# Kernel optimization log

Hardware: AMD Instinct MI355X
Metric: run time of the kernel (lower is better)

## Reference

```python
import jax, jax.numpy as jnp
import numpy as np

EMB_DIM = 1024
HEAD_DIM = 64
NUM_HEADS = EMB_DIM // HEAD_DIM  # 16
BATCH = 2
SEQ = 2048


def setup_inputs() -> dict:
    key = jax.random.key(0)
    ks = jax.random.split(key, 8)
    s = 0.02
    return {
        "q": jax.random.normal(ks[0], (BATCH, SEQ, EMB_DIM), dtype=jnp.float32),
        "k": jax.random.normal(ks[1], (BATCH, SEQ, EMB_DIM), dtype=jnp.float32),
        "v": jax.random.normal(ks[2], (BATCH, SEQ, EMB_DIM), dtype=jnp.float32),
        "W_q": jax.random.normal(ks[3], (HEAD_DIM, HEAD_DIM), dtype=jnp.float32) * s,
        "W_k": jax.random.normal(ks[4], (HEAD_DIM, HEAD_DIM), dtype=jnp.float32) * s,
        "W_v": jax.random.normal(ks[5], (HEAD_DIM, HEAD_DIM), dtype=jnp.float32) * s,
        "W_fc": jax.random.normal(ks[6], (EMB_DIM, EMB_DIM), dtype=jnp.float32) * s,
        "b_fc": jax.random.normal(ks[7], (EMB_DIM,), dtype=jnp.float32) * s,
    }


def reference(q, k, v, W_q, W_k, W_v, W_fc, b_fc):
    b = v.shape[0]
    # split into heads: [B, S, H, D]
    qh = q.reshape(b, -1, NUM_HEADS, HEAD_DIM)
    kh = k.reshape(b, -1, NUM_HEADS, HEAD_DIM)
    vh = v.reshape(b, -1, NUM_HEADS, HEAD_DIM)
    # per-head shared projections (nn.Linear: x @ W.T, no bias)
    qh = jnp.einsum('bshd,ed->bshe', qh, W_q)
    kh = jnp.einsum('bshd,ed->bshe', kh, W_k)
    vh = jnp.einsum('bshd,ed->bshe', vh, W_v)
    # scores: [B, Q, K, H]
    attn = jnp.einsum('nqhd,nkhd->nqkh', qh, kh)
    # NOTE (faithful to source): softmax over the HEADS axis (dim=3),
    # and scale by sqrt(emb_dim), not sqrt(head_dim).
    attn = jax.nn.softmax(attn / jnp.sqrt(jnp.float32(EMB_DIM)), axis=3)
    # weighted values: [B, Q, H, D] -> [B, Q, EMB]
    out = jnp.einsum('nqkh,nkhd->nqhd', attn, vh).reshape(b, -1, EMB_DIM)
    return out @ W_fc.T + b_fc
```

## Files before the change

kernel.cpp:

```cpp
#include <hip/hip_runtime.h>
#include <hip/hip_bf16.h>

#define S_LEN 2048
#define NHEAD 16
#define HDIM 64
#define EMB 1024

typedef short v8s __attribute__((ext_vector_type(8)));
typedef float v4f __attribute__((ext_vector_type(4)));

__device__ __forceinline__ float bflo(unsigned u) {
    union { unsigned u; float f; } v; v.u = u << 16; return v.f;
}
__device__ __forceinline__ float bfhi(unsigned u) {
    union { unsigned u; float f; } v; v.u = u & 0xFFFF0000u; return v.f;
}
__device__ __forceinline__ unsigned cvtpk(float lo, float hi) {
    union { __hip_bfloat162 h2; unsigned u; } v;
    float2 f; f.x = lo; f.y = hi;
    v.h2 = __float22bfloat162_rn(f);
    return v.u;
}
__device__ __forceinline__ unsigned short f2bf(float f) {
    return (unsigned short)cvtpk(f, f);
}
__device__ __forceinline__ v8s cvt8(float4 a, float4 b) {
    v8s r;
    ((unsigned*)&r)[0] = cvtpk(a.x, a.y);
    ((unsigned*)&r)[1] = cvtpk(a.z, a.w);
    ((unsigned*)&r)[2] = cvtpk(b.x, b.y);
    ((unsigned*)&r)[3] = cvtpk(b.z, b.w);
    return r;
}

__global__ __launch_bounds__(128) void k_proj2(
    const float* __restrict__ q, const float* __restrict__ k, const float* __restrict__ v,
    const float* __restrict__ Wq, const float* __restrict__ Wk, const float* __restrict__ Wv,
    unsigned short* __restrict__ Qp, unsigned short* __restrict__ Kp, unsigned short* __restrict__ Vt)
{
    __shared__ unsigned short Tq[2][16][72];
    const int t = threadIdx.x, wave = t >> 6, lane = t & 63;
    const int l15 = lane & 15, l4 = lane >> 4;
    const int mtx = blockIdx.y;
    const int hq = blockIdx.z;
    const int row0 = blockIdx.x * 32 + wave * 16;
    const int b = row0 >> 11, s0 = row0 & 2047;
    const float* X = (mtx == 0) ? q : (mtx == 1) ? k : v;
    const float* W = (mtx == 0) ? Wq : (mtx == 1) ? Wk : Wv;

    v8s wf[4][2];
    #pragma unroll
    for (int tile = 0; tile < 4; ++tile)
        #pragma unroll
        for (int c2 = 0; c2 < 2; ++c2) {
            const float* wp = W + (tile * 16 + l15) * 64 + c2 * 32 + l4 * 8;
            wf[tile][c2] = cvt8(*(const float4*)wp, *(const float4*)(wp + 4));
        }

    #pragma unroll
    for (int hi = 0; hi < 4; ++hi) {
        const int h = hq * 4 + hi;
        v8s xf[2];
        #pragma unroll
        for (int c2 = 0; c2 < 2; ++c2) {
            const float* xp = X + (size_t)(row0 + l15) * EMB + h * 64 + c2 * 32 + l4 * 8;
            xf[c2] = cvt8(*(const float4*)xp, *(const float4*)(xp + 4));
        }
        v4f acc[4];
        #pragma unroll
        for (int i = 0; i < 4; ++i) acc[i] = (v4f){0.f, 0.f, 0.f, 0.f};
        if (mtx < 2) {
            #pragma unroll
            for (int ns = 0; ns < 4; ++ns)
                #pragma unroll
                for (int c2 = 0; c2 < 2; ++c2)
                    acc[ns] = __builtin_amdgcn_mfma_f32_16x16x32_bf16(xf[c2], wf[ns][c2], acc[ns], 0, 0, 0);
            #pragma unroll
            for (int ns = 0; ns < 4; ++ns)
                #pragma unroll
                for (int r = 0; r < 4; ++r)
                    Tq[wave][l4 * 4 + r][ns * 16 + l15] = f2bf(acc[ns][r]);
            const int row = lane >> 2, c8 = (lane & 3) * 16;
            uint4 d0 = *(const uint4*)&Tq[wave][row][c8];
            uint4 d1 = *(const uint4*)&Tq[wave][row][c8 + 8];
            unsigned short* dst = ((mtx == 0) ? Qp : Kp)
                + (size_t)(b * NHEAD + h) * S_LEN * HDIM + (size_t)(s0 + row) * HDIM + c8;
            *(uint4*)dst = d0;
            *(uint4*)(dst + 8) = d1;
        } else {
            #pragma unroll
            for (int ms = 0; ms < 4; ++ms)
                #pragma unroll
                for (int c2 = 0; c2 < 2; ++c2)
                    acc[ms] = __builtin_amdgcn_mfma_f32_16x16x32_bf16(wf[ms][c2], xf[c2], acc[ms], 0, 0, 0);
            unsigned short* dst = Vt + (size_t)(b * NHEAD + h) * HDIM * S_LEN;
            #pragma unroll
            for (int ms = 0; ms < 4; ++ms)
                #pragma unroll
                for (int r = 0; r < 4; ++r)
                    dst[(size_t)(ms * 16 + l4 * 4 + r) * S_LEN + s0 + l15] = f2bf(acc[ms][r]);
        }
    }
}

__global__ __launch_bounds__(256) void k_cvtw(
    const float* __restrict__ W, unsigned short* __restrict__ Wb)
{
    const int i = (blockIdx.x * 256 + threadIdx.x) * 4;
    float4 wv = *(const float4*)(W + i);
    uint2 pk;
    pk.x = cvtpk(wv.x, wv.y);
    pk.y = cvtpk(wv.z, wv.w);
    *(uint2*)(Wb + i) = pk;
}

__global__ __launch_bounds__(1024, 4) void k_fattn(
    const unsigned short* __restrict__ Qp, const unsigned short* __restrict__ Kp,
    const unsigned short* __restrict__ Vt, unsigned short* __restrict__ Op)
{
    __shared__ unsigned short Pex[16][64][40];
    __shared__ unsigned ZrsU[64][20];
    const int t = threadIdx.x, wave = t >> 6, lane = t & 63;
    const int l15 = lane & 15, l4 = lane >> 4;
    const int h = wave;
    const int id = blockIdx.x;
    const int slot = id & 7;
    const int kqb = slot & 3;
    const int bsel = slot >> 2;
    const int qt = bsel * 32 + (id >> 3);
    const int b = qt >> 5;
    const int q0 = (qt & 31) * 64;
    const unsigned short* qh = Qp + (size_t)(b * NHEAD + h) * S_LEN * HDIM;
    const unsigned short* kh = Kp + (size_t)(b * NHEAD + h) * S_LEN * HDIM;
    const unsigned short* vh = Vt + (size_t)(b * NHEAD + h) * HDIM * S_LEN;

    v8s aq[4][2];
    #pragma unroll
    for (int qs = 0; qs < 4; ++qs)
        #pragma unroll
        for (int c2 = 0; c2 < 2; ++c2)
            aq[qs][c2] = *(const v8s*)(qh + (size_t)(q0 + qs * 16 + l15) * HDIM + c2 * 32 + l4 * 8);

    v4f o[4][4];
    #pragma unroll
    for (int qs = 0; qs < 4; ++qs)
        #pragma unroll
        for (int ds = 0; ds < 4; ++ds)
            o[qs][ds] = (v4f){0.f, 0.f, 0.f, 0.f};

    const int zq = t >> 4;
    const int zc = t & 15;

    for (int c = 0; c < 16; ++c) {
        const int kk0 = kqb * 512 + c * 32;
        #pragma unroll
        for (int ks = 0; ks < 2; ++ks) {
            const unsigned short* kb = kh + (size_t)(kk0 + ks * 16 + l15) * HDIM + l4 * 8;
            v8s b0 = *(const v8s*)kb;
            v8s b1 = *(const v8s*)(kb + 32);
            #pragma unroll
            for (int qs = 0; qs < 4; ++qs) {
                v4f sf = (v4f){0.f, 0.f, 0.f, 0.f};
                sf = __builtin_amdgcn_mfma_f32_16x16x32_bf16(aq[qs][0], b0, sf, 0, 0, 0);
                sf = __builtin_amdgcn_mfma_f32_16x16x32_bf16(aq[qs][1], b1, sf, 0, 0, 0);
                const int rb = qs * 16 + l4 * 4;
                unsigned p01 = cvtpk(__expf(sf[0] * 0.03125f), __expf(sf[1] * 0.03125f));
                unsigned p23 = cvtpk(__expf(sf[2] * 0.03125f), __expf(sf[3] * 0.03125f));
                Pex[h][rb + 0][ks * 16 + l15] = (unsigned short)p01;
                Pex[h][rb + 1][ks * 16 + l15] = (unsigned short)(p01 >> 16);
                Pex[h][rb + 2][ks * 16 + l15] = (unsigned short)p23;
                Pex[h][rb + 3][ks * 16 + l15] = (unsigned short)(p23 >> 16);
            }
        }
        __syncthreads();
        {
            float z0 = 0.f, z1 = 0.f;
            #pragma unroll
            for (int hh = 0; hh < 16; ++hh) {
                unsigned u = *(const unsigned*)&Pex[hh][zq][zc * 2];
                z0 += bflo(u); z1 += bfhi(u);
            }
            ZrsU[zq][zc] = cvtpk(__builtin_amdgcn_rcpf(z0), __builtin_amdgcn_rcpf(z1));
        }
        __syncthreads();
        {
            v8s bv[4];
            #pragma unroll
            for (int ds = 0; ds < 4; ++ds)
                bv[ds] = *(const v8s*)(vh + (size_t)(ds * 16 + l15) * S_LEN + kk0 + l4 * 8);
            #pragma unroll
            for (int qs = 0; qs < 4; ++qs) {
                uint4 pu = *(const uint4*)&Pex[h][qs * 16 + l15][l4 * 8];
                uint4 zv = *(const uint4*)&ZrsU[qs * 16 + l15][l4 * 4];
                v8s pn;
                ((unsigned*)&pn)[0] = cvtpk(bflo(pu.x) * bflo(zv.x), bfhi(pu.x) * bfhi(zv.x));
                ((unsigned*)&pn)[1] = cvtpk(bflo(pu.y) * bflo(zv.y), bfhi(pu.y) * bfhi(zv.y));
                ((unsigned*)&pn)[2] = cvtpk(bflo(pu.z) * bflo(zv.z), bfhi(pu.z) * bfhi(zv.z));
                ((unsigned*)&pn)[3] = cvtpk(bflo(pu.w) * bflo(zv.w), bfhi(pu.w) * bfhi(zv.w));
                #pragma unroll
                for (int ds = 0; ds < 4; ++ds)
                    o[qs][ds] = __builtin_amdgcn_mfma_f32_16x16x32_bf16(pn, bv[ds], o[qs][ds], 0, 0, 0);
            }
        }
    }

    unsigned short* op = Op + (size_t)(kqb * 2 + b) * S_LEN * EMB;
    #pragma unroll
    for (int qs = 0; qs < 4; ++qs)
        #pragma unroll
        for (int ds = 0; ds < 4; ++ds)
            #pragma unroll
            for (int r = 0; r < 4; ++r)
                op[(size_t)(q0 + qs * 16 + l4 * 4 + r) * EMB + h * 64 + ds * 16 + l15] =
                    f2bf(o[qs][ds][r]);
}

__global__ __launch_bounds__(256) void k_merge4(
    const unsigned short* __restrict__ Op, unsigned short* __restrict__ AO)
{
    const size_t i = ((size_t)blockIdx.x * 256 + threadIdx.x) * 8;
    const size_t row = i >> 10;
    const int b = (int)(row >> 11);
    const size_t off = (row & 2047) * EMB + (i & 1023);
    float a0 = 0, a1 = 0, a2 = 0, a3 = 0, a4 = 0, a5 = 0, a6 = 0, a7 = 0;
    #pragma unroll
    for (int kq = 0; kq < 4; ++kq) {
        uint4 u = *(const uint4*)(Op + (size_t)(kq * 2 + b) * S_LEN * EMB + off);
        a0 += bflo(u.x); a1 += bfhi(u.x);
        a2 += bflo(u.y); a3 += bfhi(u.y);
        a4 += bflo(u.z); a5 += bfhi(u.z);
        a6 += bflo(u.w); a7 += bfhi(u.w);
    }
    uint4 r;
    r.x = cvtpk(a0, a1); r.y = cvtpk(a2, a3);
    r.z = cvtpk(a4, a5); r.w = cvtpk(a6, a7);
    *(uint4*)(AO + i) = r;
}

__global__ __launch_bounds__(256) void k_fc(
    const unsigned short* __restrict__ AO, const unsigned short* __restrict__ Wb,
    const float* __restrict__ bias, float* __restrict__ out)
{
    const int t = threadIdx.x, wave = t >> 6, lane = t & 63;
    const int l15 = lane & 15, l4 = lane >> 4;
    const int m0 = blockIdx.x * 128 + wave * 32;
    const int n0 = blockIdx.y * 64;
    v4f c[2][4];
    #pragma unroll
    for (int i = 0; i < 2; ++i)
        #pragma unroll
        for (int j = 0; j < 4; ++j) c[i][j] = (v4f){0.f, 0.f, 0.f, 0.f};
    for (int k = 0; k < EMB; k += 32) {
        v8s a0 = *(const v8s*)(AO + (size_t)(m0 + l15) * EMB + k + l4 * 8);
        v8s a1 = *(const v8s*)(AO + (size_t)(m0 + 16 + l15) * EMB + k + l4 * 8);
        #pragma unroll
        for (int ns = 0; ns < 4; ++ns) {
            v8s bw = *(const v8s*)(Wb + (size_t)(n0 + ns * 16 + l15) * EMB + k + l4 * 8);
            c[0][ns] = __builtin_amdgcn_mfma_f32_16x16x32_bf16(a0, bw, c[0][ns], 0, 0, 0);
            c[1][ns] = __builtin_amdgcn_mfma_f32_16x16x32_bf16(a1, bw, c[1][ns], 0, 0, 0);
        }
    }
    #pragma unroll
    for (int ms = 0; ms < 2; ++ms)
        #pragma unroll
        for (int ns = 0; ns < 4; ++ns) {
            const float bv = bias[n0 + ns * 16 + l15];
            #pragma unroll
            for (int r = 0; r < 4; ++r)
                out[(size_t)(m0 + ms * 16 + l4 * 4 + r) * EMB + n0 + ns * 16 + l15] = c[ms][ns][r] + bv;
        }
}

extern "C" void kernel_launch(void* const* d_in, const int* in_sizes, int n_in,
                              void* d_out, int out_size, void* d_ws, size_t ws_size,
                              hipStream_t stream)
{
    (void)in_sizes; (void)n_in; (void)out_size; (void)ws_size;
    const float* q   = (const float*)d_in[0];
    const float* k   = (const float*)d_in[1];
    const float* v   = (const float*)d_in[2];
    const float* Wq  = (const float*)d_in[3];
    const float* Wk  = (const float*)d_in[4];
    const float* Wv  = (const float*)d_in[5];
    const float* Wfc = (const float*)d_in[6];
    const float* bfc = (const float*)d_in[7];

    char* w = (char*)d_ws;
    unsigned short* Qp = (unsigned short*)(w);
    unsigned short* Kp = (unsigned short*)(w + (8u  << 20));
    unsigned short* Vt = (unsigned short*)(w + (16u << 20));
    unsigned short* Wb = (unsigned short*)(w + (24u << 20));
    unsigned short* Op = (unsigned short*)(w + (26u << 20));
    unsigned short* AO = Qp;

    k_proj2 <<<dim3(128, 3, 4), dim3(128),  0, stream>>>(q, k, v, Wq, Wk, Wv, Qp, Kp, Vt);
    k_cvtw  <<<dim3(1024),      dim3(256),  0, stream>>>(Wfc, Wb);
    k_fattn <<<dim3(256),       dim3(1024), 0, stream>>>(Qp, Kp, Vt, Op);
    k_merge4<<<dim3(2048),      dim3(256),  0, stream>>>(Op, AO);
    k_fc    <<<dim3(32, 16),    dim3(256),  0, stream>>>(AO, Wb, bfc, (float*)d_out);
}
```

Baseline: 277.7 us.

## Transpose MFMA operands, swizzle packed P layout, and stage output stores through LDS

Swaps the MFMA operand order so each lane holds four consecutive query rows per key column. The exponentiated scores can then be written as packed uint2 words in a swizzled LDS layout instead of four scalar 16-bit stores. The head-sum normalization now reads contiguous uint2 per thread and processes four values. The key chunk grows from 32 to 64, halving the number of barrier pairs. The epilogue stages bf16 outputs through LDS so global writes become coalesced 16-byte stores instead of scattered 2-byte stores. The trade-off is more LDS per block and more complex index arithmetic.

```diff
diff --git a/kernel.cpp b/kernel.cpp
--- a/kernel.cpp
+++ b/kernel.cpp
@@ -118,8 +118,9 @@
     const unsigned short* __restrict__ Qp, const unsigned short* __restrict__ Kp,
     const unsigned short* __restrict__ Vt, unsigned short* __restrict__ Op)
 {
-    __shared__ unsigned short Pex[16][64][40];
-    __shared__ unsigned ZrsU[64][20];
+    __shared__ uint2 LDSU[18432];
+    uint2* PexF = LDSU;
+    uint2* ZrF  = LDSU + 16384;
     const int t = threadIdx.x, wave = t >> 6, lane = t & 63;
     const int l15 = lane & 15, l4 = lane >> 4;
     const int h = wave;
@@ -148,71 +149,88 @@
         for (int ds = 0; ds < 4; ++ds)
             o[qs][ds] = (v4f){0.f, 0.f, 0.f, 0.f};
 
-    const int zq = t >> 4;
-    const int zc = t & 15;
-
-    for (int c = 0; c < 16; ++c) {
-        const int kk0 = kqb * 512 + c * 32;
-        #pragma unroll
-        for (int ks = 0; ks < 2; ++ks) {
+    uint2* myP = PexF + h * 1024;
+    const float SC = 0.03125f;
+
+    for (int c = 0; c < 8; ++c) {
+        const int kk0 = kqb * 512 + c * 64;
+        #pragma unroll
+        for (int ks = 0; ks < 4; ++ks) {
             const unsigned short* kb = kh + (size_t)(kk0 + ks * 16 + l15) * HDIM + l4 * 8;
-            v8s b0 = *(const v8s*)kb;
-            v8s b1 = *(const v8s*)(kb + 32);
+            v8s ka0 = *(const v8s*)kb;
+            v8s ka1 = *(const v8s*)(kb + 32);
+            const int wcol = l4 * 16 + ((l15 + l4 * 4 + ks * 8) & 15);
             #pragma unroll
             for (int qs = 0; qs < 4; ++qs) {
                 v4f sf = (v4f){0.f, 0.f, 0.f, 0.f};
-                sf = __builtin_amdgcn_mfma_f32_16x16x32_bf16(aq[qs][0], b0, sf, 0, 0, 0);
-                sf = __builtin_amdgcn_mfma_f32_16x16x32_bf16(aq[qs][1], b1, sf, 0, 0, 0);
-                const int rb = qs * 16 + l4 * 4;
-                unsigned p01 = cvtpk(__expf(sf[0] * 0.03125f), __expf(sf[1] * 0.03125f));
-                unsigned p23 = cvtpk(__expf(sf[2] * 0.03125f), __expf(sf[3] * 0.03125f));
-                Pex[h][rb + 0][ks * 16 + l15] = (unsigned short)p01;
-                Pex[h][rb + 1][ks * 16 + l15] = (unsigned short)(p01 >> 16);
-                Pex[h][rb + 2][ks * 16 + l15] = (unsigned short)p23;
-                Pex[h][rb + 3][ks * 16 + l15] = (unsigned short)(p23 >> 16);
+                sf = __builtin_amdgcn_mfma_f32_16x16x32_bf16(ka0, aq[qs][0], sf, 0, 0, 0);
+                sf = __builtin_amdgcn_mfma_f32_16x16x32_bf16(ka1, aq[qs][1], sf, 0, 0, 0);
+                uint2 pe;
+                pe.x = cvtpk(__expf(sf[0] * SC), __expf(sf[1] * SC));
+                pe.y = cvtpk(__expf(sf[2] * SC), __expf(sf[3] * SC));
+                myP[(qs * 4 + ks) * 64 + wcol] = pe;
             }
         }
         __syncthreads();
         {
-            float z0 = 0.f, z1 = 0.f;
-            #pragma unroll
-            for (int hh = 0; hh < 16; ++hh) {
-                unsigned u = *(const unsigned*)&Pex[hh][zq][zc * 2];
-                z0 += bflo(u); z1 += bfhi(u);
+            uint2 u = PexF[t];
+            float z0 = bflo(u.x), z1 = bfhi(u.x), z2 = bflo(u.y), z3 = bfhi(u.y);
+            #pragma unroll
+            for (int hh = 1; hh < 16; ++hh) {
+                u = PexF[hh * 1024 + t];
+                z0 += bflo(u.x); z1 += bfhi(u.x); z2 += bflo(u.y); z3 += bfhi(u.y);
             }
-            ZrsU[zq][zc] = cvtpk(__builtin_amdgcn_rcpf(z0), __builtin_amdgcn_rcpf(z1));
+            uint2 zo;
+            zo.x = cvtpk(__builtin_amdgcn_rcpf(z0), __builtin_amdgcn_rcpf(z1));
+            zo.y = cvtpk(__builtin_amdgcn_rcpf(z2), __builtin_amdgcn_rcpf(z3));
+            ZrF[t] = zo;
         }
         __syncthreads();
-        {
+        #pragma unroll
+        for (int kp = 0; kp < 2; ++kp) {
             v8s bv[4];
             #pragma unroll
             for (int ds = 0; ds < 4; ++ds)
-                bv[ds] = *(const v8s*)(vh + (size_t)(ds * 16 + l15) * S_LEN + kk0 + l4 * 8);
+                bv[ds] = *(const v8s*)(vh + (size_t)(ds * 16 + l15) * S_LEN + kk0 + kp * 32 + l4 * 8);
+            const int ks_s = kp * 2 + (l4 >> 1);
+            const int rg0 = (l4 & 1) * 2;
+            const int i0 = ks_s * 64 + rg0 * 16 + ((l15 + rg0 * 4 + ks_s * 8) & 15);
+            const int i1 = ks_s * 64 + (rg0 + 1) * 16 + ((l15 + (rg0 + 1) * 4 + ks_s * 8) & 15);
             #pragma unroll
             for (int qs = 0; qs < 4; ++qs) {
-                uint4 pu = *(const uint4*)&Pex[h][qs * 16 + l15][l4 * 8];
-                uint4 zv = *(const uint4*)&ZrsU[qs * 16 + l15][l4 * 4];
+                const int base = qs * 256;
+                uint2 pa = myP[base + i0], pb = myP[base + i1];
+                uint2 za = ZrF[base + i0], zb = ZrF[base + i1];
                 v8s pn;
-                ((unsigned*)&pn)[0] = cvtpk(bflo(pu.x) * bflo(zv.x), bfhi(pu.x) * bfhi(zv.x));
-                ((unsigned*)&pn)[1] = cvtpk(bflo(pu.y) * bflo(zv.y), bfhi(pu.y) * bfhi(zv.y));
-                ((unsigned*)&pn)[2] = cvtpk(bflo(pu.z) * bflo(zv.z), bfhi(pu.z) * bfhi(zv.z));
-                ((unsigned*)&pn)[3] = cvtpk(bflo(pu.w) * bflo(zv.w), bfhi(pu.w) * bfhi(zv.w));
+                ((unsigned*)&pn)[0] = cvtpk(bflo(pa.x) * bflo(za.x), bfhi(pa.x) * bfhi(za.x));
+                ((unsigned*)&pn)[1] = cvtpk(bflo(pa.y) * bflo(za.y), bfhi(pa.y) * bfhi(za.y));
+                ((unsigned*)&pn)[2] = cvtpk(bflo(pb.x) * bflo(zb.x), bfhi(pb.x) * bfhi(zb.x));
+                ((unsigned*)&pn)[3] = cvtpk(bflo(pb.y) * bflo(zb.y), bfhi(pb.y) * bfhi(zb.y));
                 #pragma unroll
                 for (int ds = 0; ds < 4; ++ds)
-                    o[qs][ds] = __builtin_amdgcn_mfma_f32_16x16x32_bf16(pn, bv[ds], o[qs][ds], 0, 0, 0);
+                    o[qs][ds] = __builtin_amdgcn_mfma_f32_16x16x32_bf16(bv[ds], pn, o[qs][ds], 0, 0, 0);
             }
         }
     }
 
-    unsigned short* op = Op + (size_t)(kqb * 2 + b) * S_LEN * EMB;
+    __syncthreads();
+    uint2* myE = LDSU + h * 1152;
     #pragma unroll
     for (int qs = 0; qs < 4; ++qs)
         #pragma unroll
-        for (int ds = 0; ds < 4; ++ds)
-            #pragma unroll
-            for (int r = 0; r < 4; ++r)
-                op[(size_t)(q0 + qs * 16 + l4 * 4 + r) * EMB + h * 64 + ds * 16 + l15] =
-                    f2bf(o[qs][ds][r]);
+        for (int ds = 0; ds < 4; ++ds) {
+            uint2 wv;
+            wv.x = cvtpk(o[qs][ds][0], o[qs][ds][1]);
+            wv.y = cvtpk(o[qs][ds][2], o[qs][ds][3]);
+            myE[(qs * 16 + l15) * 18 + ds * 4 + l4] = wv;
+        }
+    unsigned short* op = Op + (size_t)(kqb * 2 + b) * S_LEN * EMB + (size_t)q0 * EMB + h * 64;
+    #pragma unroll
+    for (int it = 0; it < 8; ++it) {
+        const int qr = it * 8 + (lane >> 3);
+        uint4 dv = *(const uint4*)&myE[qr * 18 + (lane & 7) * 2];
+        *(uint4*)(op + (size_t)qr * EMB + (lane & 7) * 8) = dv;
+    }
 }
 
 __global__ __launch_bounds__(256) void k_merge4(
```

Result: slower. 347.5 us (+25.1%).

## Transpose score MFMA and pack P tiles for vectorized LDS stores

Applied to the files above, without the earlier changes.

The QK^T MFMA now puts K as the A operand and Q as B, so each lane holds four consecutive key columns for one query row. The exp values can then be written to shared memory as one 8-byte store instead of four scattered 2-byte stores. The head-sum reduction now runs on 512 threads, each summing four columns via uint2 loads, and the normalisation reads use the new packed layout. The V projection also stages its output through shared memory so global stores to the transposed Vt are 8-byte writes rather than scattered 2-byte writes. The risk is LDS bank conflicts in the new layout and half the threads sitting idle during the reduction.

```diff
diff --git a/kernel.cpp b/kernel.cpp
--- a/kernel.cpp
+++ b/kernel.cpp
@@ -38,7 +38,7 @@
     const float* __restrict__ Wq, const float* __restrict__ Wk, const float* __restrict__ Wv,
     unsigned short* __restrict__ Qp, unsigned short* __restrict__ Kp, unsigned short* __restrict__ Vt)
 {
-    __shared__ unsigned short Tq[2][16][72];
+    __shared__ unsigned short Tb[2][1280];
     const int t = threadIdx.x, wave = t >> 6, lane = t & 63;
     const int l15 = lane & 15, l4 = lane >> 4;
     const int mtx = blockIdx.y;
@@ -79,10 +79,10 @@
             for (int ns = 0; ns < 4; ++ns)
                 #pragma unroll
                 for (int r = 0; r < 4; ++r)
-                    Tq[wave][l4 * 4 + r][ns * 16 + l15] = f2bf(acc[ns][r]);
+                    Tb[wave][(l4 * 4 + r) * 72 + ns * 16 + l15] = f2bf(acc[ns][r]);
             const int row = lane >> 2, c8 = (lane & 3) * 16;
-            uint4 d0 = *(const uint4*)&Tq[wave][row][c8];
-            uint4 d1 = *(const uint4*)&Tq[wave][row][c8 + 8];
+            uint4 d0 = *(const uint4*)&Tb[wave][row * 72 + c8];
+            uint4 d1 = *(const uint4*)&Tb[wave][row * 72 + c8 + 8];
             unsigned short* dst = ((mtx == 0) ? Qp : Kp)
                 + (size_t)(b * NHEAD + h) * S_LEN * HDIM + (size_t)(s0 + row) * HDIM + c8;
             *(uint4*)dst = d0;
@@ -93,12 +93,18 @@
                 #pragma unroll
                 for (int c2 = 0; c2 < 2; ++c2)
                     acc[ms] = __builtin_amdgcn_mfma_f32_16x16x32_bf16(wf[ms][c2], xf[c2], acc[ms], 0, 0, 0);
-            unsigned short* dst = Vt + (size_t)(b * NHEAD + h) * HDIM * S_LEN;
             #pragma unroll
             for (int ms = 0; ms < 4; ++ms)
                 #pragma unroll
                 for (int r = 0; r < 4; ++r)
-                    dst[(size_t)(ms * 16 + l4 * 4 + r) * S_LEN + s0 + l15] = f2bf(acc[ms][r]);
+                    Tb[wave][(ms * 16 + l4 * 4 + r) * 20 + l15] = f2bf(acc[ms][r]);
+            unsigned short* dst = Vt + (size_t)(b * NHEAD + h) * HDIM * S_LEN + s0;
+            #pragma unroll
+            for (int it = 0; it < 4; ++it) {
+                const int dr = it * 16 + (lane >> 2), cc = (lane & 3) * 4;
+                uint2 dv = *(const uint2*)&Tb[wave][dr * 20 + cc];
+                *(uint2*)(dst + (size_t)dr * S_LEN + cc) = dv;
+            }
         }
     }
 }
@@ -118,8 +124,8 @@
     const unsigned short* __restrict__ Qp, const unsigned short* __restrict__ Kp,
     const unsigned short* __restrict__ Vt, unsigned short* __restrict__ Op)
 {
-    __shared__ unsigned short Pex[16][64][40];
-    __shared__ unsigned ZrsU[64][20];
+    __shared__ uint2 PexU[16][640];
+    __shared__ uint2 ZrU[640];
     const int t = threadIdx.x, wave = t >> 6, lane = t & 63;
     const int l15 = lane & 15, l4 = lane >> 4;
     const int h = wave;
@@ -148,39 +154,41 @@
         for (int ds = 0; ds < 4; ++ds)
             o[qs][ds] = (v4f){0.f, 0.f, 0.f, 0.f};
 
-    const int zq = t >> 4;
-    const int zc = t & 15;
+    uint2* myP = &PexU[h][0];
+    const float SC = 0.03125f;
 
     for (int c = 0; c < 16; ++c) {
         const int kk0 = kqb * 512 + c * 32;
         #pragma unroll
         for (int ks = 0; ks < 2; ++ks) {
             const unsigned short* kb = kh + (size_t)(kk0 + ks * 16 + l15) * HDIM + l4 * 8;
-            v8s b0 = *(const v8s*)kb;
-            v8s b1 = *(const v8s*)(kb + 32);
+            v8s ka0 = *(const v8s*)kb;
+            v8s ka1 = *(const v8s*)(kb + 32);
             #pragma unroll
             for (int qs = 0; qs < 4; ++qs) {
                 v4f sf = (v4f){0.f, 0.f, 0.f, 0.f};
-                sf = __builtin_amdgcn_mfma_f32_16x16x32_bf16(aq[qs][0], b0, sf, 0, 0, 0);
-                sf = __builtin_amdgcn_mfma_f32_16x16x32_bf16(aq[qs][1], b1, sf, 0, 0, 0);
-                const int rb = qs * 16 + l4 * 4;
-                unsigned p01 = cvtpk(__expf(sf[0] * 0.03125f), __expf(sf[1] * 0.03125f));
-                unsigned p23 = cvtpk(__expf(sf[2] * 0.03125f), __expf(sf[3] * 0.03125f));
-                Pex[h][rb + 0][ks * 16 + l15] = (unsigned short)p01;
-                Pex[h][rb + 1][ks * 16 + l15] = (unsigned short)(p01 >> 16);
-                Pex[h][rb + 2][ks * 16 + l15] = (unsigned short)p23;
-                Pex[h][rb + 3][ks * 16 + l15] = (unsigned short)(p23 >> 16);
+                sf = __builtin_amdgcn_mfma_f32_16x16x32_bf16(ka0, aq[qs][0], sf, 0, 0, 0);
+                sf = __builtin_amdgcn_mfma_f32_16x16x32_bf16(ka1, aq[qs][1], sf, 0, 0, 0);
+                uint2 pe;
+                pe.x = cvtpk(__expf(sf[0] * SC), __expf(sf[1] * SC));
+                pe.y = cvtpk(__expf(sf[2] * SC), __expf(sf[3] * SC));
+                myP[(qs * 16 + l15) * 10 + ks * 4 + l4] = pe;
             }
         }
         __syncthreads();
-        {
-            float z0 = 0.f, z1 = 0.f;
-            #pragma unroll
-            for (int hh = 0; hh < 16; ++hh) {
-                unsigned u = *(const unsigned*)&Pex[hh][zq][zc * 2];
-                z0 += bflo(u); z1 += bfhi(u);
+        if (t < 512) {
+            const int idx = (t >> 3) * 10 + (t & 7);
+            uint2 u = PexU[0][idx];
+            float z0 = bflo(u.x), z1 = bfhi(u.x), z2 = bflo(u.y), z3 = bfhi(u.y);
+            #pragma unroll
+            for (int hh = 1; hh < 16; ++hh) {
+                u = PexU[hh][idx];
+                z0 += bflo(u.x); z1 += bfhi(u.x); z2 += bflo(u.y); z3 += bfhi(u.y);
             }
-            ZrsU[zq][zc] = cvtpk(__builtin_amdgcn_rcpf(z0), __builtin_amdgcn_rcpf(z1));
+            uint2 zo;
+            zo.x = cvtpk(__builtin_amdgcn_rcpf(z0), __builtin_amdgcn_rcpf(z1));
+            zo.y = cvtpk(__builtin_amdgcn_rcpf(z2), __builtin_amdgcn_rcpf(z3));
+            ZrU[idx] = zo;
         }
         __syncthreads();
         {
@@ -190,8 +198,9 @@
                 bv[ds] = *(const v8s*)(vh + (size_t)(ds * 16 + l15) * S_LEN + kk0 + l4 * 8);
             #pragma unroll
             for (int qs = 0; qs < 4; ++qs) {
-                uint4 pu = *(const uint4*)&Pex[h][qs * 16 + l15][l4 * 8];
-                uint4 zv = *(const uint4*)&ZrsU[qs * 16 + l15][l4 * 4];
+                const int base = (qs * 16 + l15) * 10 + l4 * 2;
+                uint4 pu = *(const uint4*)&myP[base];
+                uint4 zv = *(const uint4*)&ZrU[base];
                 v8s pn;
                 ((unsigned*)&pn)[0] = cvtpk(bflo(pu.x) * bflo(zv.x), bfhi(pu.x) * bfhi(zv.x));
                 ((unsigned*)&pn)[1] = cvtpk(bflo(pu.y) * bflo(zv.y), bfhi(pu.y) * bfhi(zv.y));
```

New measurement: 343.7 us. 1.24x slower.
